# Kernel optimization log

Hardware: AMD Instinct MI355X
Metric: run time of the kernel (lower is better)

## Reference

```python
import jax, jax.numpy as jnp
import numpy as np

N = 50000          # num nodes
E = 800000         # num edges (before self-loops)
F_IN = 128         # num_node_features
HEADS = 8          # num_heads (layer 1)
F_HEAD = 16        # features_per_head
N_CLASSES = 32     # num_classes (layer 2, heads=1)
NEG_SLOPE = 0.2    # PyG GATConv default LeakyReLU slope


def setup_inputs() -> dict:
    key = jax.random.key(0)
    ks = jax.random.split(key, 9)
    x = jax.random.normal(ks[0], (N, F_IN), jnp.float32)
    src = jax.random.randint(ks[1], (E,), 0, N, dtype=jnp.int32)
    dst = jax.random.randint(ks[2], (E,), 0, N, dtype=jnp.int32)
    # layer 1 params
    W1 = jax.random.normal(ks[3], (F_IN, HEADS * F_HEAD), jnp.float32) / np.sqrt(F_IN).astype(np.float32)
    a_src1 = jax.random.normal(ks[4], (HEADS, F_HEAD), jnp.float32) * 0.1
    a_dst1 = jax.random.normal(ks[5], (HEADS, F_HEAD), jnp.float32) * 0.1
    b1 = jnp.zeros((HEADS * F_HEAD,), jnp.float32)  # bias_init = zeros_
    # layer 2 params (heads=1)
    W2 = jax.random.normal(ks[6], (HEADS * F_HEAD, N_CLASSES), jnp.float32) / np.sqrt(HEADS * F_HEAD).astype(np.float32)
    a_src2 = jax.random.normal(ks[7], (1, N_CLASSES), jnp.float32) * 0.1
    a_dst2 = jax.random.normal(ks[8], (1, N_CLASSES), jnp.float32) * 0.1
    b2 = jnp.zeros((N_CLASSES,), jnp.float32)
    return {"x": x, "src": src, "dst": dst,
            "W1": W1, "a_src1": a_src1, "a_dst1": a_dst1, "b1": b1,
            "W2": W2, "a_src2": a_src2, "a_dst2": a_dst2, "b2": b2}


def gat_conv(x, src, dst, W, a_src, a_dst, b, heads, feat):
    """PyG-style GATConv (concat=True, add_self_loops=True)."""
    h = (x @ W).reshape(N, heads, feat)                 # [N,H,F]
    al_src = jnp.sum(h * a_src, axis=-1)                # [N,H]
    al_dst = jnp.sum(h * a_dst, axis=-1)                # [N,H]
    loop = jnp.arange(N, dtype=src.dtype)
    s = jnp.concatenate([src, loop])                    # [E+N]
    d = jnp.concatenate([dst, loop])                    # [E+N]
    e = jax.nn.leaky_relu(al_src[s] + al_dst[d], NEG_SLOPE)   # [E+N,H]
    # numerically stable softmax over edges grouped by dst node
    m = jax.ops.segment_max(e, d, num_segments=N)       # [N,H]
    ex = jnp.exp(e - m[d])
    denom = jax.ops.segment_sum(ex, d, num_segments=N)  # [N,H]
    alpha = ex / denom[d]                               # [E+N,H]
    out = jax.ops.segment_sum(alpha[:, :, None] * h[s], d, num_segments=N)  # [N,H,F]
    return out.reshape(N, heads * feat) + b


def reference(x, src, dst, W1, a_src1, a_dst1, b1, W2, a_src2, a_dst2, b2):
    h = gat_conv(x, src, dst, W1, a_src1, a_dst1, b1, HEADS, F_HEAD)
    h = jax.nn.elu(h)
    h = gat_conv(h, src, dst, W2, a_src2, a_dst2, b2, 1, N_CLASSES)
    return jax.nn.log_softmax(h, axis=1)
```

## Files before the change

kernel.cpp:

```cpp
#include <hip/hip_runtime.h>

#define N_NODES   50000
#define N_EDGES   800000
#define NEG_SLOPE 0.2f
#define NBKT      256
#define NPB       196
#define EPB       3125
#define CAP       4096
#define G1BLK     782

typedef float f32x2 __attribute__((ext_vector_type(2)));
typedef float f32x4 __attribute__((ext_vector_type(4)));

__device__ __forceinline__ float leaky(float x) {
    return x > 0.f ? x : x * NEG_SLOPE;
}

__device__ __forceinline__ unsigned short f2bf(float f) {
    unsigned int u = __float_as_uint(f);
    unsigned int r = (u + 0x7FFFu + ((u >> 16) & 1u)) >> 16;
    return (unsigned short)r;
}

__device__ __forceinline__ unsigned int pack2bf(float a, float b) {
    return (unsigned int)f2bf(a) | ((unsigned int)f2bf(b) << 16);
}

__device__ __forceinline__ f32x2 bf2x2(unsigned int p) {
    f32x2 r;
    r.x = __uint_as_float(p << 16);
    r.y = __uint_as_float(p & 0xFFFF0000u);
    return r;
}

__device__ __forceinline__ f32x2 lo2(f32x4 v) { return __builtin_shufflevector(v, v, 0, 1); }
__device__ __forceinline__ f32x2 hi2(f32x4 v) { return __builtin_shufflevector(v, v, 2, 3); }

__device__ __forceinline__ void pkfma_lo(f32x2& acc, f32x2 a, f32x2 w) {
    asm("v_pk_fma_f32 %0, %1, %2, %0 op_sel:[0,0,0] op_sel_hi:[0,1,1]"
        : "+v"(acc) : "v"(a), "v"(w));
}
__device__ __forceinline__ void pkfma_hi(f32x2& acc, f32x2 a, f32x2 w) {
    asm("v_pk_fma_f32 %0, %1, %2, %0 op_sel:[1,0,0] op_sel_hi:[1,1,1]"
        : "+v"(acc) : "v"(a), "v"(w));
}
__device__ __forceinline__ f32x2 plow(float x) {
    f32x2 r;
    asm("" : "=v"(r));
    r.x = x;
    return r;
}

__global__ __launch_bounds__(256) void k_bin_gemm1(
    const int* __restrict__ src, const int* __restrict__ dst,
    int* __restrict__ cursor_g, unsigned int* __restrict__ binned,
    const float* __restrict__ x, const float* __restrict__ W1,
    const float* __restrict__ a_src, const float* __restrict__ a_dst,
    unsigned short* __restrict__ h1b, float* __restrict__ al_src,
    float* __restrict__ al_dst)
{
    __shared__ __align__(16) unsigned char smem[49152];
    const int tid = threadIdx.x;

    if (blockIdx.x < NBKT) {
        int* dstc = (int*)smem;
        int* cnt  = (int*)(smem + 12512);
        int* cur  = (int*)(smem + 13536);
        const int blk = blockIdx.x;
        const int e0  = blk * EPB;
        cnt[tid] = 0;
        __syncthreads();
        for (int j = tid; j < EPB; j += 256) {
            int d = dst[e0 + j];
            dstc[j] = d;
            atomicAdd(&cnt[d / NPB], 1);
        }
        __syncthreads();
        const int c = cnt[tid];
        int base = c ? atomicAdd(&cursor_g[tid], c) : 0;
        cur[tid] = tid * CAP + base;
        __syncthreads();
        for (int j = tid; j < EPB; j += 256) {
            int d   = dstc[j];
            int bkt = d / NPB;
            int dl  = d - bkt * NPB;
            int pos = atomicAdd(&cur[bkt], 1);
            binned[pos] = (unsigned int)src[e0 + j] | ((unsigned int)dl << 18);
        }
        return;
    }

    uint2* xs = (uint2*)smem;
    uint2* ws = (uint2*)(smem + 16384);
    const int bid  = (int)blockIdx.x - NBKT;
    const int row0 = bid * 64;
    const int tc   = tid & 31;
    const int tr   = tid >> 5;
    const float4* x4  = (const float4*)x;
    const float4* W14 = (const float4*)W1;

    #pragma unroll
    for (int p = 0; p < 8; ++p) {
        int i = tid + p * 256;
        int r = i >> 5, g = i & 31;
        int gr = row0 + r; if (gr > N_NODES - 1) gr = N_NODES - 1;
        float4 v = x4[gr * 32 + g];
        xs[r * 32 + g] = make_uint2(pack2bf(v.x, v.y), pack2bf(v.z, v.w));
    }
    #pragma unroll
    for (int p = 0; p < 16; ++p) {
        int i = tid + p * 256;
        int k = i >> 5, cg = i & 31;
        float4 v = W14[k * 32 + cg];
        ws[k * 32 + cg] = make_uint2(pack2bf(v.x, v.y), pack2bf(v.z, v.w));
    }
    __syncthreads();

    f32x2 acc[8][2];
    #pragma unroll
    for (int i = 0; i < 8; ++i) {
        acc[i][0] = (f32x2){0.f, 0.f};
        acc[i][1] = (f32x2){0.f, 0.f};
    }

    for (int k4 = 0; k4 < 32; ++k4) {
        f32x2 aP[8][2];
        #pragma unroll
        for (int i = 0; i < 8; ++i) {
            uint2 q = xs[(tr * 8 + i) * 32 + k4];
            aP[i][0] = bf2x2(q.x);
            aP[i][1] = bf2x2(q.y);
        }
        #pragma unroll
        for (int kk = 0; kk < 4; ++kk) {
            uint2 qw = ws[(k4 * 4 + kk) * 32 + tc];
            f32x2 wlo = bf2x2(qw.x);
            f32x2 whi = bf2x2(qw.y);
            #pragma unroll
            for (int i = 0; i < 8; ++i) {
                f32x2 ap = aP[i][kk >> 1];
                if ((kk & 1) == 0) {
                    pkfma_lo(acc[i][0], ap, wlo);
                    pkfma_lo(acc[i][1], ap, whi);
                } else {
                    pkfma_hi(acc[i][0], ap, wlo);
                    pkfma_hi(acc[i][1], ap, whi);
                }
            }
        }
    }

    const int head = tc >> 2;
    const float4 as4 = ((const float4*)a_src)[tc];
    const float4 ad4 = ((const float4*)a_dst)[tc];
    #pragma unroll
    for (int i = 0; i < 8; ++i) {
        int r = row0 + tr * 8 + i;
        float s = acc[i][0].x * as4.x + acc[i][0].y * as4.y
                + acc[i][1].x * as4.z + acc[i][1].y * as4.w;
        float d = acc[i][0].x * ad4.x + acc[i][0].y * ad4.y
                + acc[i][1].x * ad4.z + acc[i][1].y * ad4.w;
        s += __shfl_xor(s, 1); s += __shfl_xor(s, 2);
        d += __shfl_xor(d, 1); d += __shfl_xor(d, 2);
        if (r < N_NODES) {
            ((uint2*)h1b)[r * 32 + tc] =
                make_uint2(pack2bf(acc[i][0].x, acc[i][0].y),
                           pack2bf(acc[i][1].x, acc[i][1].y));
            if ((tc & 3) == 0) {
                al_src[r * 8 + head] = s;
                al_dst[r * 8 + head] = d;
            }
        }
    }
}

__global__ __launch_bounds__(1024) void k_csr_fine(const unsigned int* __restrict__ binned,
                                                   const int* __restrict__ cursor_g,
                                                   int* __restrict__ row_beg,
                                                   int* __restrict__ row_end,
                                                   int* __restrict__ csr) {
    __shared__ int cnt[256];
    __shared__ int cur[256];
    __shared__ int wsum[4];
    const int b = blockIdx.x, tid = threadIdx.x;
    const int start = b * CAP;
    const int nE    = cursor_g[b];
    if (tid < 256) cnt[tid] = 0;
    __syncthreads();
    for (int j = tid; j < nE; j += 1024)
        atomicAdd(&cnt[(binned[start + j] >> 18) & 255], 1);
    __syncthreads();
    int v = 0;
    if (tid < 256) v = cnt[tid];
    int sv = v;
    #pragma unroll
    for (int off = 1; off < 64; off <<= 1) {
        int t = __shfl_up(sv, off);
        if ((tid & 63) >= off) sv += t;
    }
    if (tid < 256 && (tid & 63) == 63) wsum[tid >> 6] = sv;
    __syncthreads();
    if (tid < 256) {
        int w = tid >> 6;
        int add = 0;
        #pragma unroll
        for (int i = 0; i < 3; ++i) add += (i < w) ? wsum[i] : 0;
        int excl = sv + add - v;
        cur[tid] = excl;
        const int node = b * NPB + tid;
        if (tid < NPB && node < N_NODES) {
            row_beg[node] = start + excl;
            row_end[node] = start + excl + v;
        }
    }
    __syncthreads();
    for (int j = tid; j < nE; j += 1024) {
        unsigned int p = binned[start + j];
        int dl  = (p >> 18) & 255;
        int pos = start + atomicAdd(&cur[dl], 1);
        csr[pos] = (int)(p & 0x3FFFFu);
    }
}

__global__ __launch_bounds__(256) void k_agg1g2(
    const unsigned short* __restrict__ h1b, const float* __restrict__ al_src,
    const float* __restrict__ al_dst, const int* __restrict__ row_beg,
    const int* __restrict__ row_end, const int* __restrict__ csr_src,
    const float* __restrict__ b1, const float* __restrict__ W2,
    const float* __restrict__ a_src2, const float* __restrict__ a_dst2,
    unsigned short* __restrict__ t2b, float* __restrict__ alS2,
    float* __restrict__ alD2)
{
    __shared__ __align__(16) float w2s[128 * 32];
    __shared__ __align__(16) float h2row[4][128];
    const int tid  = threadIdx.x;
    const int wv   = tid >> 6;
    const int n    = blockIdx.x * 4 + wv;
    const int l    = tid & 63;
    const int slot = l >> 4;
    const int f2   = l & 15;
    const int head = f2 >> 1;
    const uint4* h1q = (const uint4*)h1b;

    float4 wreg[4];
    {
        const float4* W2v = (const float4*)W2;
        #pragma unroll
        for (int p = 0; p < 4; ++p) wreg[p] = W2v[tid + p * 256];
    }
    const float alD = al_dst[n * 8 + head];
    const int beg = row_beg[n], end = row_end[n];
    {
        float4* w2sv = (float4*)w2s;
        #pragma unroll
        for (int p = 0; p < 4; ++p) {
            int g = tid + p * 256;
            w2sv[g ^ ((g >> 7) & 7)] = wreg[p];
        }
    }
    __syncthreads();

    float denom = 0.f;
    f32x2 a01 = {0.f, 0.f}, a23 = {0.f, 0.f}, a45 = {0.f, 0.f}, a67 = {0.f, 0.f};

    if (slot == 0) {
        float w = __expf(leaky(al_src[n * 8 + head] + alD));
        uint4 q = h1q[n * 16 + f2];
        denom = w;
        f32x2 wp = plow(w);
        pkfma_lo(a01, wp, bf2x2(q.x));
        pkfma_lo(a23, wp, bf2x2(q.y));
        pkfma_lo(a45, wp, bf2x2(q.z));
        pkfma_lo(a67, wp, bf2x2(q.w));
    }

    for (int j = beg + slot; j < end; j += 16) {
        const int e1 = (j + 4  < end) ? j + 4  : j;
        const int e2 = (j + 8  < end) ? j + 8  : j;
        const int e3 = (j + 12 < end) ? j + 12 : j;
        int s0 = csr_src[j];
        int s1 = csr_src[e1];
        int s2 = csr_src[e2];
        int s3 = csr_src[e3];
        float l0 = al_src[s0 * 8 + head];
        float l1 = al_src[s1 * 8 + head];
        float l2 = al_src[s2 * 8 + head];
        float l3 = al_src[s3 * 8 + head];
        uint4 q0 = h1q[s0 * 16 + f2];
        uint4 q1 = h1q[s1 * 16 + f2];
        uint4 q2 = h1q[s2 * 16 + f2];
        uint4 q3 = h1q[s3 * 16 + f2];
        float w0 = __expf(leaky(l0 + alD));
        float w1 = __expf(leaky(l1 + alD)); w1 = (e1 != j) ? w1 : 0.f;
        float w2 = __expf(leaky(l2 + alD)); w2 = (e2 != j) ? w2 : 0.f;
        float w3 = __expf(leaky(l3 + alD)); w3 = (e3 != j) ? w3 : 0.f;
        denom += (w0 + w1) + (w2 + w3);
        f32x2 wA; wA.x = w0; wA.y = w1;
        f32x2 wB; wB.x = w2; wB.y = w3;
        pkfma_lo(a01, wA, bf2x2(q0.x));
        pkfma_lo(a23, wA, bf2x2(q0.y));
        pkfma_lo(a45, wA, bf2x2(q0.z));
        pkfma_lo(a67, wA, bf2x2(q0.w));
        pkfma_hi(a01, wA, bf2x2(q1.x));
        pkfma_hi(a23, wA, bf2x2(q1.y));
        pkfma_hi(a45, wA, bf2x2(q1.z));
        pkfma_hi(a67, wA, bf2x2(q1.w));
        pkfma_lo(a01, wB, bf2x2(q2.x));
        pkfma_lo(a23, wB, bf2x2(q2.y));
        pkfma_lo(a45, wB, bf2x2(q2.z));
        pkfma_lo(a67, wB, bf2x2(q2.w));
        pkfma_hi(a01, wB, bf2x2(q3.x));
        pkfma_hi(a23, wB, bf2x2(q3.y));
        pkfma_hi(a45, wB, bf2x2(q3.z));
        pkfma_hi(a67, wB, bf2x2(q3.w));
    }

    #pragma unroll
    for (int off = 16; off <= 32; off <<= 1) {
        a01.x += __shfl_xor(a01.x, off); a01.y += __shfl_xor(a01.y, off);
        a23.x += __shfl_xor(a23.x, off); a23.y += __shfl_xor(a23.y, off);
        a45.x += __shfl_xor(a45.x, off); a45.y += __shfl_xor(a45.y, off);
        a67.x += __shfl_xor(a67.x, off); a67.y += __shfl_xor(a67.y, off);
        denom += __shfl_xor(denom, off);
    }

    {
        const float4 bA = ((const float4*)b1)[f2 * 2];
        const float4 bB = ((const float4*)b1)[f2 * 2 + 1];
        float inv = 1.f / denom;
        float o[8];
        o[0] = a01.x * inv + bA.x; o[1] = a01.y * inv + bA.y;
        o[2] = a23.x * inv + bA.z; o[3] = a23.y * inv + bA.w;
        o[4] = a45.x * inv + bB.x; o[5] = a45.y * inv + bB.y;
        o[6] = a67.x * inv + bB.z; o[7] = a67.y * inv + bB.w;
        #pragma unroll
        for (int i = 0; i < 8; ++i) o[i] = o[i] > 0.f ? o[i] : expm1f(o[i]);
        if (slot == 0) {
            *(float4*)&h2row[wv][f2 * 8]     = make_float4(o[0], o[1], o[2], o[3]);
            *(float4*)&h2row[wv][f2 * 8 + 4] = make_float4(o[4], o[5], o[6], o[7]);
        }
    }

    const int cg = l & 7;
    const int kg = l >> 3;
    const float* hrow = h2row[wv];
    f32x4 hv[4];
    #pragma unroll
    for (int t = 0; t < 4; ++t)
        hv[t] = *(const f32x4*)&hrow[kg * 16 + t * 4];
    const f32x4* w2v = (const f32x4*)w2s;
    f32x2 s01 = {0.f, 0.f}, s23 = {0.f, 0.f};
    #pragma unroll
    for (int t = 0; t < 4; ++t) {
        f32x2 hlo = lo2(hv[t]);
        f32x2 hhi = hi2(hv[t]);
        #pragma unroll
        for (int u = 0; u < 4; ++u) {
            const int k = kg * 16 + t * 4 + u;
            f32x4 w4 = w2v[(k * 8 + cg) ^ kg];
            f32x2 wlo = lo2(w4);
            f32x2 whi = hi2(w4);
            if (u == 0)      { pkfma_lo(s01, hlo, wlo); pkfma_lo(s23, hlo, whi); }
            else if (u == 1) { pkfma_hi(s01, hlo, wlo); pkfma_hi(s23, hlo, whi); }
            else if (u == 2) { pkfma_lo(s01, hhi, wlo); pkfma_lo(s23, hhi, whi); }
            else             { pkfma_hi(s01, hhi, wlo); pkfma_hi(s23, hhi, whi); }
        }
    }
    #pragma unroll
    for (int off = 8; off <= 32; off <<= 1) {
        s01.x += __shfl_xor(s01.x, off); s01.y += __shfl_xor(s01.y, off);
        s23.x += __shfl_xor(s23.x, off); s23.y += __shfl_xor(s23.y, off);
    }

    if (l < 8)
        ((uint2*)t2b)[n * 8 + cg] =
            make_uint2(pack2bf(s01.x, s01.y), pack2bf(s23.x, s23.y));

    const float4 as2 = ((const float4*)a_src2)[cg];
    const float4 ad2 = ((const float4*)a_dst2)[cg];
    float s2 = s01.x * as2.x + s01.y * as2.y + s23.x * as2.z + s23.y * as2.w;
    float d2 = s01.x * ad2.x + s01.y * ad2.y + s23.x * ad2.z + s23.y * ad2.w;
    #pragma unroll
    for (int off = 1; off <= 4; off <<= 1) {
        s2 += __shfl_xor(s2, off);
        d2 += __shfl_xor(d2, off);
    }
    if (l == 0) {
        alS2[n] = s2;
        alD2[n] = d2;
    }
}

__global__ __launch_bounds__(256) void k_agg2(
    const unsigned short* __restrict__ t2b, const float* __restrict__ al_src,
    const float* __restrict__ al_dst, const int* __restrict__ row_beg,
    const int* __restrict__ row_end, const int* __restrict__ csr_src,
    const float* __restrict__ b2, float* __restrict__ out)
{
    const int n = blockIdx.x * 4 + (threadIdx.x >> 6);
    const int l = threadIdx.x & 63;
    const int slot = l >> 3;
    const int f4   = l & 7;
    const uint2* t2u = (const uint2*)t2b;

    const float alD = al_dst[n];
    const int beg = row_beg[n], end = row_end[n];
    float denom = 0.f;
    f32x2 a01 = {0.f, 0.f}, a23 = {0.f, 0.f};
    if (slot == 0) {
        float w = __expf(leaky(al_src[n] + alD));
        uint2 q = t2u[n * 8 + f4];
        denom = w;
        f32x2 wp = plow(w);
        pkfma_lo(a01, wp, bf2x2(q.x));
        pkfma_lo(a23, wp, bf2x2(q.y));
    }
    for (int j = beg + slot; j < end; j += 32) {
        const int e1 = (j + 8  < end) ? j + 8  : j;
        const int e2 = (j + 16 < end) ? j + 16 : j;
        const int e3 = (j + 24 < end) ? j + 24 : j;
        int s0 = csr_src[j];
        int s1 = csr_src[e1];
        int s2 = csr_src[e2];
        int s3 = csr_src[e3];
        float l0 = al_src[s0];
        float l1 = al_src[s1];
        float l2 = al_src[s2];
        float l3 = al_src[s3];
        uint2 q0 = t2u[s0 * 8 + f4];
        uint2 q1 = t2u[s1 * 8 + f4];
        uint2 q2 = t2u[s2 * 8 + f4];
        uint2 q3 = t2u[s3 * 8 + f4];
        float w0 = __expf(leaky(l0 + alD));
        float w1 = __expf(leaky(l1 + alD)); w1 = (e1 != j) ? w1 : 0.f;
        float w2 = __expf(leaky(l2 + alD)); w2 = (e2 != j) ? w2 : 0.f;
        float w3 = __expf(leaky(l3 + alD)); w3 = (e3 != j) ? w3 : 0.f;
        denom += (w0 + w1) + (w2 + w3);
        f32x2 wA; wA.x = w0; wA.y = w1;
        f32x2 wB; wB.x = w2; wB.y = w3;
        pkfma_lo(a01, wA, bf2x2(q0.x));
        pkfma_lo(a23, wA, bf2x2(q0.y));
        pkfma_hi(a01, wA, bf2x2(q1.x));
        pkfma_hi(a23, wA, bf2x2(q1.y));
        pkfma_lo(a01, wB, bf2x2(q2.x));
        pkfma_lo(a23, wB, bf2x2(q2.y));
        pkfma_hi(a01, wB, bf2x2(q3.x));
        pkfma_hi(a23, wB, bf2x2(q3.y));
    }
    #pragma unroll
    for (int off = 8; off <= 32; off <<= 1) {
        a01.x += __shfl_xor(a01.x, off); a01.y += __shfl_xor(a01.y, off);
        a23.x += __shfl_xor(a23.x, off); a23.y += __shfl_xor(a23.y, off);
        denom += __shfl_xor(denom, off);
    }

    const float4 bb = ((const float4*)b2)[f4];
    float inv = 1.f / denom;
    float o0 = a01.x * inv + bb.x;
    float o1 = a01.y * inv + bb.y;
    float o2 = a23.x * inv + bb.z;
    float o3 = a23.y * inv + bb.w;
    float m = fmaxf(fmaxf(o0, o1), fmaxf(o2, o3));
    for (int off = 1; off <= 4; off <<= 1) m = fmaxf(m, __shfl_xor(m, off));
    float ssum = __expf(o0 - m) + __expf(o1 - m) + __expf(o2 - m) + __expf(o3 - m);
    for (int off = 1; off <= 4; off <<= 1) ssum += __shfl_xor(ssum, off);
    float lg = m + __logf(ssum);
    if (slot == 0)
        ((float4*)out)[n * 8 + f4] = make_float4(o0 - lg, o1 - lg, o2 - lg, o3 - lg);
}

extern "C" void kernel_launch(void* const* d_in, const int* in_sizes, int n_in,
                              void* d_out, int out_size, void* d_ws, size_t ws_size,
                              hipStream_t stream) {
    const float* x      = (const float*)d_in[0];
    const int*   src    = (const int*)d_in[1];
    const int*   dst    = (const int*)d_in[2];
    const float* W1     = (const float*)d_in[3];
    const float* a_src1 = (const float*)d_in[4];
    const float* a_dst1 = (const float*)d_in[5];
    const float* b1     = (const float*)d_in[6];
    const float* W2     = (const float*)d_in[7];
    const float* a_src2 = (const float*)d_in[8];
    const float* a_dst2 = (const float*)d_in[9];
    const float* b2     = (const float*)d_in[10];
    float* out = (float*)d_out;

    char* ws = (char*)d_ws;
    size_t off = 0;
    auto alloc = [&](size_t bytes) {
        void* p = ws + off;
        off += (bytes + 255) & ~(size_t)255;
        return p;
    };
    unsigned short* h1b = (unsigned short*)alloc((size_t)N_NODES * 128 * 2);
    unsigned short* t2b = (unsigned short*)alloc((size_t)N_NODES * 32 * 2);
    float* alS1    = (float*)alloc((size_t)N_NODES * 8 * 4);
    float* alD1    = (float*)alloc((size_t)N_NODES * 8 * 4);
    float* alS2    = (float*)alloc((size_t)N_NODES * 4);
    float* alD2    = (float*)alloc((size_t)N_NODES * 4);
    int*   row_beg = (int*)alloc((size_t)N_NODES * 4);
    int*   row_end = (int*)alloc((size_t)N_NODES * 4);
    int*   csr     = (int*)alloc((size_t)NBKT * CAP * 4);
    unsigned int* binned = (unsigned int*)alloc((size_t)NBKT * CAP * 4);
    int*   cursor  = (int*)alloc((size_t)NBKT * 4);
    (void)ws_size; (void)in_sizes; (void)n_in; (void)out_size;

    hipMemsetAsync(cursor, 0, (size_t)NBKT * 4, stream);
    k_bin_gemm1<<<NBKT + G1BLK, 256, 0, stream>>>(
        src, dst, cursor, binned,
        x, W1, a_src1, a_dst1, h1b, alS1, alD1);
    k_csr_fine<<<NBKT, 1024, 0, stream>>>(binned, cursor, row_beg, row_end, csr);
    k_agg1g2<<<N_NODES / 4, 256, 0, stream>>>(
        h1b, alS1, alD1, row_beg, row_end, csr,
        b1, W2, a_src2, a_dst2, t2b, alS2, alD2);
    k_agg2<<<N_NODES / 4, 256, 0, stream>>>(t2b, alS2, alD2, row_beg, row_end, csr, b2, out);
}
```

Before: 202.0 us.

## Fuse all GAT stages into one persistent cooperative kernel with grid syncs

Replaces the memset plus four kernel launches with one persistent cooperative kernel. Its blocks loop over tasks (binning, GEMM1, CSR build, layer-1 aggregation with the W2 projection, layer-2 aggregation) and separate the stages with grid-wide syncs. The GEMM tile now stages W1 in four chunks so shared memory drops to 24KB, which is meant to allow more resident blocks. The aim is to remove launch gaps and the tail between stages, at the cost of grid.sync overhead, a grid size capped by occupancy, and the CSR stage now using 256 threads per block where it used 1024.

```diff
diff --git a/kernel.cpp b/kernel.cpp
--- a/kernel.cpp
+++ b/kernel.cpp
@@ -1,4 +1,7 @@
 #include <hip/hip_runtime.h>
+#include <hip/hip_cooperative_groups.h>
+
+namespace cg = cooperative_groups;
 
 #define N_NODES   50000
 #define N_EDGES   800000
@@ -8,6 +11,7 @@
 #define EPB       3125
 #define CAP       4096
 #define G1BLK     782
+#define NGRP      12500
 
 typedef float f32x2 __attribute__((ext_vector_type(2)));
 typedef float f32x4 __attribute__((ext_vector_type(4)));
@@ -51,422 +55,429 @@
     return r;
 }
 
-__global__ __launch_bounds__(256) void k_bin_gemm1(
+__global__ __launch_bounds__(256) void k_fused(
     const int* __restrict__ src, const int* __restrict__ dst,
     int* __restrict__ cursor_g, unsigned int* __restrict__ binned,
     const float* __restrict__ x, const float* __restrict__ W1,
-    const float* __restrict__ a_src, const float* __restrict__ a_dst,
-    unsigned short* __restrict__ h1b, float* __restrict__ al_src,
-    float* __restrict__ al_dst)
-{
-    __shared__ __align__(16) unsigned char smem[49152];
-    const int tid = threadIdx.x;
-
-    if (blockIdx.x < NBKT) {
-        int* dstc = (int*)smem;
-        int* cnt  = (int*)(smem + 12512);
-        int* cur  = (int*)(smem + 13536);
-        const int blk = blockIdx.x;
-        const int e0  = blk * EPB;
-        cnt[tid] = 0;
-        __syncthreads();
-        for (int j = tid; j < EPB; j += 256) {
-            int d = dst[e0 + j];
-            dstc[j] = d;
-            atomicAdd(&cnt[d / NPB], 1);
-        }
-        __syncthreads();
-        const int c = cnt[tid];
-        int base = c ? atomicAdd(&cursor_g[tid], c) : 0;
-        cur[tid] = tid * CAP + base;
-        __syncthreads();
-        for (int j = tid; j < EPB; j += 256) {
-            int d   = dstc[j];
-            int bkt = d / NPB;
-            int dl  = d - bkt * NPB;
-            int pos = atomicAdd(&cur[bkt], 1);
-            binned[pos] = (unsigned int)src[e0 + j] | ((unsigned int)dl << 18);
-        }
-        return;
-    }
-
-    uint2* xs = (uint2*)smem;
-    uint2* ws = (uint2*)(smem + 16384);
-    const int bid  = (int)blockIdx.x - NBKT;
-    const int row0 = bid * 64;
-    const int tc   = tid & 31;
-    const int tr   = tid >> 5;
-    const float4* x4  = (const float4*)x;
-    const float4* W14 = (const float4*)W1;
-
-    #pragma unroll
-    for (int p = 0; p < 8; ++p) {
-        int i = tid + p * 256;
-        int r = i >> 5, g = i & 31;
-        int gr = row0 + r; if (gr > N_NODES - 1) gr = N_NODES - 1;
-        float4 v = x4[gr * 32 + g];
-        xs[r * 32 + g] = make_uint2(pack2bf(v.x, v.y), pack2bf(v.z, v.w));
-    }
-    #pragma unroll
-    for (int p = 0; p < 16; ++p) {
-        int i = tid + p * 256;
-        int k = i >> 5, cg = i & 31;
-        float4 v = W14[k * 32 + cg];
-        ws[k * 32 + cg] = make_uint2(pack2bf(v.x, v.y), pack2bf(v.z, v.w));
-    }
-    __syncthreads();
-
-    f32x2 acc[8][2];
-    #pragma unroll
-    for (int i = 0; i < 8; ++i) {
-        acc[i][0] = (f32x2){0.f, 0.f};
-        acc[i][1] = (f32x2){0.f, 0.f};
-    }
-
-    for (int k4 = 0; k4 < 32; ++k4) {
-        f32x2 aP[8][2];
-        #pragma unroll
-        for (int i = 0; i < 8; ++i) {
-            uint2 q = xs[(tr * 8 + i) * 32 + k4];
-            aP[i][0] = bf2x2(q.x);
-            aP[i][1] = bf2x2(q.y);
-        }
-        #pragma unroll
-        for (int kk = 0; kk < 4; ++kk) {
-            uint2 qw = ws[(k4 * 4 + kk) * 32 + tc];
-            f32x2 wlo = bf2x2(qw.x);
-            f32x2 whi = bf2x2(qw.y);
-            #pragma unroll
-            for (int i = 0; i < 8; ++i) {
-                f32x2 ap = aP[i][kk >> 1];
-                if ((kk & 1) == 0) {
-                    pkfma_lo(acc[i][0], ap, wlo);
-                    pkfma_lo(acc[i][1], ap, whi);
-                } else {
-                    pkfma_hi(acc[i][0], ap, wlo);
-                    pkfma_hi(acc[i][1], ap, whi);
-                }
-            }
-        }
-    }
-
-    const int head = tc >> 2;
-    const float4 as4 = ((const float4*)a_src)[tc];
-    const float4 ad4 = ((const float4*)a_dst)[tc];
-    #pragma unroll
-    for (int i = 0; i < 8; ++i) {
-        int r = row0 + tr * 8 + i;
-        float s = acc[i][0].x * as4.x + acc[i][0].y * as4.y
-                + acc[i][1].x * as4.z + acc[i][1].y * as4.w;
-        float d = acc[i][0].x * ad4.x + acc[i][0].y * ad4.y
-                + acc[i][1].x * ad4.z + acc[i][1].y * ad4.w;
-        s += __shfl_xor(s, 1); s += __shfl_xor(s, 2);
-        d += __shfl_xor(d, 1); d += __shfl_xor(d, 2);
-        if (r < N_NODES) {
-            ((uint2*)h1b)[r * 32 + tc] =
-                make_uint2(pack2bf(acc[i][0].x, acc[i][0].y),
-                           pack2bf(acc[i][1].x, acc[i][1].y));
-            if ((tc & 3) == 0) {
-                al_src[r * 8 + head] = s;
-                al_dst[r * 8 + head] = d;
-            }
-        }
-    }
-}
-
-__global__ __launch_bounds__(1024) void k_csr_fine(const unsigned int* __restrict__ binned,
-                                                   const int* __restrict__ cursor_g,
-                                                   int* __restrict__ row_beg,
-                                                   int* __restrict__ row_end,
-                                                   int* __restrict__ csr) {
-    __shared__ int cnt[256];
-    __shared__ int cur[256];
-    __shared__ int wsum[4];
-    const int b = blockIdx.x, tid = threadIdx.x;
-    const int start = b * CAP;
-    const int nE    = cursor_g[b];
-    if (tid < 256) cnt[tid] = 0;
-    __syncthreads();
-    for (int j = tid; j < nE; j += 1024)
-        atomicAdd(&cnt[(binned[start + j] >> 18) & 255], 1);
-    __syncthreads();
-    int v = 0;
-    if (tid < 256) v = cnt[tid];
-    int sv = v;
-    #pragma unroll
-    for (int off = 1; off < 64; off <<= 1) {
-        int t = __shfl_up(sv, off);
-        if ((tid & 63) >= off) sv += t;
-    }
-    if (tid < 256 && (tid & 63) == 63) wsum[tid >> 6] = sv;
-    __syncthreads();
-    if (tid < 256) {
-        int w = tid >> 6;
-        int add = 0;
-        #pragma unroll
-        for (int i = 0; i < 3; ++i) add += (i < w) ? wsum[i] : 0;
-        int excl = sv + add - v;
-        cur[tid] = excl;
-        const int node = b * NPB + tid;
-        if (tid < NPB && node < N_NODES) {
-            row_beg[node] = start + excl;
-            row_end[node] = start + excl + v;
-        }
-    }
-    __syncthreads();
-    for (int j = tid; j < nE; j += 1024) {
-        unsigned int p = binned[start + j];
-        int dl  = (p >> 18) & 255;
-        int pos = start + atomicAdd(&cur[dl], 1);
-        csr[pos] = (int)(p & 0x3FFFFu);
-    }
-}
-
-__global__ __launch_bounds__(256) void k_agg1g2(
-    const unsigned short* __restrict__ h1b, const float* __restrict__ al_src,
-    const float* __restrict__ al_dst, const int* __restrict__ row_beg,
-    const int* __restrict__ row_end, const int* __restrict__ csr_src,
+    const float* __restrict__ a_src1, const float* __restrict__ a_dst1,
+    unsigned short* __restrict__ h1b, float* __restrict__ alS1,
+    float* __restrict__ alD1,
+    int* __restrict__ row_beg, int* __restrict__ row_end, int* __restrict__ csr,
     const float* __restrict__ b1, const float* __restrict__ W2,
     const float* __restrict__ a_src2, const float* __restrict__ a_dst2,
     unsigned short* __restrict__ t2b, float* __restrict__ alS2,
-    float* __restrict__ alD2)
+    float* __restrict__ alD2,
+    const float* __restrict__ b2, float* __restrict__ out)
 {
-    __shared__ __align__(16) float w2s[128 * 32];
-    __shared__ __align__(16) float h2row[4][128];
+    __shared__ __align__(16) unsigned char smem[24576];
+    cg::grid_group grid = cg::this_grid();
     const int tid  = threadIdx.x;
-    const int wv   = tid >> 6;
-    const int n    = blockIdx.x * 4 + wv;
-    const int l    = tid & 63;
-    const int slot = l >> 4;
-    const int f2   = l & 15;
-    const int head = f2 >> 1;
-    const uint4* h1q = (const uint4*)h1b;
-
-    float4 wreg[4];
-    {
-        const float4* W2v = (const float4*)W2;
-        #pragma unroll
-        for (int p = 0; p < 4; ++p) wreg[p] = W2v[tid + p * 256];
-    }
-    const float alD = al_dst[n * 8 + head];
-    const int beg = row_beg[n], end = row_end[n];
-    {
-        float4* w2sv = (float4*)w2s;
-        #pragma unroll
-        for (int p = 0; p < 4; ++p) {
-            int g = tid + p * 256;
-            w2sv[g ^ ((g >> 7) & 7)] = wreg[p];
+    const int bid  = blockIdx.x;
+    const int nblk = gridDim.x;
+
+    for (int i = bid * 256 + tid; i < NBKT; i += nblk * 256) cursor_g[i] = 0;
+    grid.sync();
+
+    for (int task = bid; task < NBKT + G1BLK; task += nblk) {
+        if (task < NBKT) {
+            int* dstc = (int*)smem;
+            int* cnt  = (int*)(smem + 12512);
+            int* cur  = (int*)(smem + 13536);
+            const int e0 = task * EPB;
+            __syncthreads();
+            cnt[tid] = 0;
+            __syncthreads();
+            for (int j = tid; j < EPB; j += 256) {
+                int d = dst[e0 + j];
+                dstc[j] = d;
+                atomicAdd(&cnt[d / NPB], 1);
+            }
+            __syncthreads();
+            const int c = cnt[tid];
+            int base = c ? atomicAdd(&cursor_g[tid], c) : 0;
+            cur[tid] = tid * CAP + base;
+            __syncthreads();
+            for (int j = tid; j < EPB; j += 256) {
+                int d   = dstc[j];
+                int bkt = d / NPB;
+                int dl  = d - bkt * NPB;
+                int pos = atomicAdd(&cur[bkt], 1);
+                binned[pos] = (unsigned int)src[e0 + j] | ((unsigned int)dl << 18);
+            }
+            __syncthreads();
+        } else {
+            uint2* xs = (uint2*)smem;
+            uint2* ws = (uint2*)(smem + 16384);
+            const int row0 = (task - NBKT) * 64;
+            const int tc   = tid & 31;
+            const int tr   = tid >> 5;
+            const float4* x4  = (const float4*)x;
+            const float4* W14 = (const float4*)W1;
+
+            __syncthreads();
+            #pragma unroll
+            for (int p = 0; p < 8; ++p) {
+                int i = tid + p * 256;
+                int r = i >> 5, g = i & 31;
+                int gr = row0 + r; if (gr > N_NODES - 1) gr = N_NODES - 1;
+                float4 v = x4[gr * 32 + g];
+                xs[r * 32 + g] = make_uint2(pack2bf(v.x, v.y), pack2bf(v.z, v.w));
+            }
+
+            f32x2 acc[8][2];
+            #pragma unroll
+            for (int i = 0; i < 8; ++i) {
+                acc[i][0] = (f32x2){0.f, 0.f};
+                acc[i][1] = (f32x2){0.f, 0.f};
+            }
+
+            for (int q = 0; q < 4; ++q) {
+                if (q) __syncthreads();
+                #pragma unroll
+                for (int p = 0; p < 4; ++p) {
+                    int i = tid + p * 256;
+                    int k = i >> 5, cgq = i & 31;
+                    float4 v = W14[(q * 32 + k) * 32 + cgq];
+                    ws[k * 32 + cgq] = make_uint2(pack2bf(v.x, v.y), pack2bf(v.z, v.w));
+                }
+                __syncthreads();
+                for (int k4 = 0; k4 < 8; ++k4) {
+                    f32x2 aP[8][2];
+                    #pragma unroll
+                    for (int i = 0; i < 8; ++i) {
+                        uint2 qq = xs[(tr * 8 + i) * 32 + q * 8 + k4];
+                        aP[i][0] = bf2x2(qq.x);
+                        aP[i][1] = bf2x2(qq.y);
+                    }
+                    #pragma unroll
+                    for (int kk = 0; kk < 4; ++kk) {
+                        uint2 qw = ws[(k4 * 4 + kk) * 32 + tc];
+                        f32x2 wlo = bf2x2(qw.x);
+                        f32x2 whi = bf2x2(qw.y);
+                        #pragma unroll
+                        for (int i = 0; i < 8; ++i) {
+                            f32x2 ap = aP[i][kk >> 1];
+                            if ((kk & 1) == 0) {
+                                pkfma_lo(acc[i][0], ap, wlo);
+                                pkfma_lo(acc[i][1], ap, whi);
+                            } else {
+                                pkfma_hi(acc[i][0], ap, wlo);
+                                pkfma_hi(acc[i][1], ap, whi);
+                            }
+                        }
+                    }
+                }
+            }
+
+            const int head = tc >> 2;
+            const float4 as4 = ((const float4*)a_src1)[tc];
+            const float4 ad4 = ((const float4*)a_dst1)[tc];
+            #pragma unroll
+            for (int i = 0; i < 8; ++i) {
+                int r = row0 + tr * 8 + i;
+                float s = acc[i][0].x * as4.x + acc[i][0].y * as4.y
+                        + acc[i][1].x * as4.z + acc[i][1].y * as4.w;
+                float d = acc[i][0].x * ad4.x + acc[i][0].y * ad4.y
+                        + acc[i][1].x * ad4.z + acc[i][1].y * ad4.w;
+                s += __shfl_xor(s, 1); s += __shfl_xor(s, 2);
+                d += __shfl_xor(d, 1); d += __shfl_xor(d, 2);
+                if (r < N_NODES) {
+                    ((uint2*)h1b)[r * 32 + tc] =
+                        make_uint2(pack2bf(acc[i][0].x, acc[i][0].y),
+                                   pack2bf(acc[i][1].x, acc[i][1].y));
+                    if ((tc & 3) == 0) {
+                        alS1[r * 8 + head] = s;
+                        alD1[r * 8 + head] = d;
+                    }
+                }
+            }
+            __syncthreads();
         }
     }
-    __syncthreads();
-
-    float denom = 0.f;
-    f32x2 a01 = {0.f, 0.f}, a23 = {0.f, 0.f}, a45 = {0.f, 0.f}, a67 = {0.f, 0.f};
-
-    if (slot == 0) {
-        float w = __expf(leaky(al_src[n * 8 + head] + alD));
-        uint4 q = h1q[n * 16 + f2];
-        denom = w;
-        f32x2 wp = plow(w);
-        pkfma_lo(a01, wp, bf2x2(q.x));
-        pkfma_lo(a23, wp, bf2x2(q.y));
-        pkfma_lo(a45, wp, bf2x2(q.z));
-        pkfma_lo(a67, wp, bf2x2(q.w));
-    }
-
-    for (int j = beg + slot; j < end; j += 16) {
-        const int e1 = (j + 4  < end) ? j + 4  : j;
-        const int e2 = (j + 8  < end) ? j + 8  : j;
-        const int e3 = (j + 12 < end) ? j + 12 : j;
-        int s0 = csr_src[j];
-        int s1 = csr_src[e1];
-        int s2 = csr_src[e2];
-        int s3 = csr_src[e3];
-        float l0 = al_src[s0 * 8 + head];
-        float l1 = al_src[s1 * 8 + head];
-        float l2 = al_src[s2 * 8 + head];
-        float l3 = al_src[s3 * 8 + head];
-        uint4 q0 = h1q[s0 * 16 + f2];
-        uint4 q1 = h1q[s1 * 16 + f2];
-        uint4 q2 = h1q[s2 * 16 + f2];
-        uint4 q3 = h1q[s3 * 16 + f2];
-        float w0 = __expf(leaky(l0 + alD));
-        float w1 = __expf(leaky(l1 + alD)); w1 = (e1 != j) ? w1 : 0.f;
-        float w2 = __expf(leaky(l2 + alD)); w2 = (e2 != j) ? w2 : 0.f;
-        float w3 = __expf(leaky(l3 + alD)); w3 = (e3 != j) ? w3 : 0.f;
-        denom += (w0 + w1) + (w2 + w3);
-        f32x2 wA; wA.x = w0; wA.y = w1;
-        f32x2 wB; wB.x = w2; wB.y = w3;
-        pkfma_lo(a01, wA, bf2x2(q0.x));
-        pkfma_lo(a23, wA, bf2x2(q0.y));
-        pkfma_lo(a45, wA, bf2x2(q0.z));
-        pkfma_lo(a67, wA, bf2x2(q0.w));
-        pkfma_hi(a01, wA, bf2x2(q1.x));
-        pkfma_hi(a23, wA, bf2x2(q1.y));
-        pkfma_hi(a45, wA, bf2x2(q1.z));
-        pkfma_hi(a67, wA, bf2x2(q1.w));
-        pkfma_lo(a01, wB, bf2x2(q2.x));
-        pkfma_lo(a23, wB, bf2x2(q2.y));
-        pkfma_lo(a45, wB, bf2x2(q2.z));
-        pkfma_lo(a67, wB, bf2x2(q2.w));
-        pkfma_hi(a01, wB, bf2x2(q3.x));
-        pkfma_hi(a23, wB, bf2x2(q3.y));
-        pkfma_hi(a45, wB, bf2x2(q3.z));
-        pkfma_hi(a67, wB, bf2x2(q3.w));
-    }
-
-    #pragma unroll
-    for (int off = 16; off <= 32; off <<= 1) {
-        a01.x += __shfl_xor(a01.x, off); a01.y += __shfl_xor(a01.y, off);
-        a23.x += __shfl_xor(a23.x, off); a23.y += __shfl_xor(a23.y, off);
-        a45.x += __shfl_xor(a45.x, off); a45.y += __shfl_xor(a45.y, off);
-        a67.x += __shfl_xor(a67.x, off); a67.y += __shfl_xor(a67.y, off);
-        denom += __shfl_xor(denom, off);
-    }
+    grid.sync();
 
     {
-        const float4 bA = ((const float4*)b1)[f2 * 2];
-        const float4 bB = ((const float4*)b1)[f2 * 2 + 1];
-        float inv = 1.f / denom;
-        float o[8];
-        o[0] = a01.x * inv + bA.x; o[1] = a01.y * inv + bA.y;
-        o[2] = a23.x * inv + bA.z; o[3] = a23.y * inv + bA.w;
-        o[4] = a45.x * inv + bB.x; o[5] = a45.y * inv + bB.y;
-        o[6] = a67.x * inv + bB.z; o[7] = a67.y * inv + bB.w;
-        #pragma unroll
-        for (int i = 0; i < 8; ++i) o[i] = o[i] > 0.f ? o[i] : expm1f(o[i]);
-        if (slot == 0) {
-            *(float4*)&h2row[wv][f2 * 8]     = make_float4(o[0], o[1], o[2], o[3]);
-            *(float4*)&h2row[wv][f2 * 8 + 4] = make_float4(o[4], o[5], o[6], o[7]);
+        int* cnt  = (int*)smem;
+        int* cur  = (int*)(smem + 1024);
+        int* wsum = (int*)(smem + 2048);
+        for (int b = bid; b < NBKT; b += nblk) {
+            const int start = b * CAP;
+            const int nE    = cursor_g[b];
+            __syncthreads();
+            cnt[tid] = 0;
+            __syncthreads();
+            for (int j = tid; j < nE; j += 256)
+                atomicAdd(&cnt[(binned[start + j] >> 18) & 255], 1);
+            __syncthreads();
+            const int v = cnt[tid];
+            int sv = v;
+            #pragma unroll
+            for (int off = 1; off < 64; off <<= 1) {
+                int t = __shfl_up(sv, off);
+                if ((tid & 63) >= off) sv += t;
+            }
+            if ((tid & 63) == 63) wsum[tid >> 6] = sv;
+            __syncthreads();
+            {
+                int w = tid >> 6;
+                int add = 0;
+                #pragma unroll
+                for (int i = 0; i < 3; ++i) add += (i < w) ? wsum[i] : 0;
+                int excl = sv + add - v;
+                cur[tid] = excl;
+                const int node = b * NPB + tid;
+                if (tid < NPB && node < N_NODES) {
+                    row_beg[node] = start + excl;
+                    row_end[node] = start + excl + v;
+                }
+            }
+            __syncthreads();
+            for (int j = tid; j < nE; j += 256) {
+                unsigned int p = binned[start + j];
+                int dl  = (p >> 18) & 255;
+                int pos = start + atomicAdd(&cur[dl], 1);
+                csr[pos] = (int)(p & 0x3FFFFu);
+            }
         }
     }
-
-    const int cg = l & 7;
-    const int kg = l >> 3;
-    const float* hrow = h2row[wv];
-    f32x4 hv[4];
-    #pragma unroll
-    for (int t = 0; t < 4; ++t)
-        hv[t] = *(const f32x4*)&hrow[kg * 16 + t * 4];
-    const f32x4* w2v = (const f32x4*)w2s;
-    f32x2 s01 = {0.f, 0.f}, s23 = {0.f, 0.f};
-    #pragma unroll
-    for (int t = 0; t < 4; ++t) {
-        f32x2 hlo = lo2(hv[t]);
-        f32x2 hhi = hi2(hv[t]);
-        #pragma unroll
-        for (int u = 0; u < 4; ++u) {
-            const int k = kg * 16 + t * 4 + u;
-            f32x4 w4 = w2v[(k * 8 + cg) ^ kg];
-            f32x2 wlo = lo2(w4);
-            f32x2 whi = hi2(w4);
-            if (u == 0)      { pkfma_lo(s01, hlo, wlo); pkfma_lo(s23, hlo, whi); }
-            else if (u == 1) { pkfma_hi(s01, hlo, wlo); pkfma_hi(s23, hlo, whi); }
-            else if (u == 2) { pkfma_lo(s01, hhi, wlo); pkfma_lo(s23, hhi, whi); }
-            else             { pkfma_hi(s01, hhi, wlo); pkfma_hi(s23, hhi, whi); }
+    grid.sync();
+
+    {
+        float* w2s = (float*)smem;
+        float (*h2row)[128] = (float(*)[128])(smem + 16384);
+        const int wv   = tid >> 6;
+        const int l    = tid & 63;
+        const int slot = l >> 4;
+        const int f2   = l & 15;
+        const int head = f2 >> 1;
+        const int cg   = l & 7;
+        const int kg   = l >> 3;
+        const uint4* h1q = (const uint4*)h1b;
+
+        __syncthreads();
+        {
+            const float4* W2v = (const float4*)W2;
+            float4* w2sv = (float4*)w2s;
+            #pragma unroll
+            for (int p = 0; p < 4; ++p) {
+                int g = tid + p * 256;
+                w2sv[g ^ ((g >> 7) & 7)] = W2v[g];
+            }
+        }
+        __syncthreads();
+
+        const float4 bA  = ((const float4*)b1)[f2 * 2];
+        const float4 bB  = ((const float4*)b1)[f2 * 2 + 1];
+        const float4 as2 = ((const float4*)a_src2)[cg];
+        const float4 ad2 = ((const float4*)a_dst2)[cg];
+        const f32x4* w2v = (const f32x4*)w2s;
+
+        for (int grp = bid; grp < NGRP; grp += nblk) {
+            const int n = grp * 4 + wv;
+            const float alD = alD1[n * 8 + head];
+            const int beg = row_beg[n], end = row_end[n];
+
+            float denom = 0.f;
+            f32x2 a01 = {0.f, 0.f}, a23 = {0.f, 0.f}, a45 = {0.f, 0.f}, a67 = {0.f, 0.f};
+
+            if (slot == 0) {
+                float w = __expf(leaky(alS1[n * 8 + head] + alD));
+                uint4 q = h1q[n * 16 + f2];
+                denom = w;
+                f32x2 wp = plow(w);
+                pkfma_lo(a01, wp, bf2x2(q.x));
+                pkfma_lo(a23, wp, bf2x2(q.y));
+                pkfma_lo(a45, wp, bf2x2(q.z));
+                pkfma_lo(a67, wp, bf2x2(q.w));
+            }
+
+            for (int j = beg + slot; j < end; j += 16) {
+                const int e1 = (j + 4  < end) ? j + 4  : j;
+                const int e2 = (j + 8  < end) ? j + 8  : j;
+                const int e3 = (j + 12 < end) ? j + 12 : j;
+                int s0 = csr[j];
+                int s1 = csr[e1];
+                int s2 = csr[e2];
+                int s3 = csr[e3];
+                float l0 = alS1[s0 * 8 + head];
+                float l1 = alS1[s1 * 8 + head];
+                float l2 = alS1[s2 * 8 + head];
+                float l3 = alS1[s3 * 8 + head];
+                uint4 q0 = h1q[s0 * 16 + f2];
+                uint4 q1 = h1q[s1 * 16 + f2];
+                uint4 q2 = h1q[s2 * 16 + f2];
+                uint4 q3 = h1q[s3 * 16 + f2];
+                float w0 = __expf(leaky(l0 + alD));
+                float w1 = __expf(leaky(l1 + alD)); w1 = (e1 != j) ? w1 : 0.f;
+                float w2 = __expf(leaky(l2 + alD)); w2 = (e2 != j) ? w2 : 0.f;
+                float w3 = __expf(leaky(l3 + alD)); w3 = (e3 != j) ? w3 : 0.f;
+                denom += (w0 + w1) + (w2 + w3);
+                f32x2 wA; wA.x = w0; wA.y = w1;
+                f32x2 wB; wB.x = w2; wB.y = w3;
+                pkfma_lo(a01, wA, bf2x2(q0.x));
+                pkfma_lo(a23, wA, bf2x2(q0.y));
+                pkfma_lo(a45, wA, bf2x2(q0.z));
+                pkfma_lo(a67, wA, bf2x2(q0.w));
+                pkfma_hi(a01, wA, bf2x2(q1.x));
+                pkfma_hi(a23, wA, bf2x2(q1.y));
+                pkfma_hi(a45, wA, bf2x2(q1.z));
+                pkfma_hi(a67, wA, bf2x2(q1.w));
+                pkfma_lo(a01, wB, bf2x2(q2.x));
+                pkfma_lo(a23, wB, bf2x2(q2.y));
+                pkfma_lo(a45, wB, bf2x2(q2.z));
+                pkfma_lo(a67, wB, bf2x2(q2.w));
+                pkfma_hi(a01, wB, bf2x2(q3.x));
+                pkfma_hi(a23, wB, bf2x2(q3.y));
+                pkfma_hi(a45, wB, bf2x2(q3.z));
+                pkfma_hi(a67, wB, bf2x2(q3.w));
+            }
+
+            #pragma unroll
+            for (int off = 16; off <= 32; off <<= 1) {
+                a01.x += __shfl_xor(a01.x, off); a01.y += __shfl_xor(a01.y, off);
+                a23.x += __shfl_xor(a23.x, off); a23.y += __shfl_xor(a23.y, off);
+                a45.x += __shfl_xor(a45.x, off); a45.y += __shfl_xor(a45.y, off);
+                a67.x += __shfl_xor(a67.x, off); a67.y += __shfl_xor(a67.y, off);
+                denom += __shfl_xor(denom, off);
+            }
+
+            {
+                float inv = 1.f / denom;
+                float o[8];
+                o[0] = a01.x * inv + bA.x; o[1] = a01.y * inv + bA.y;
+                o[2] = a23.x * inv + bA.z; o[3] = a23.y * inv + bA.w;
+                o[4] = a45.x * inv + bB.x; o[5] = a45.y * inv + bB.y;
+                o[6] = a67.x * inv + bB.z; o[7] = a67.y * inv + bB.w;
+                #pragma unroll
+                for (int i = 0; i < 8; ++i) o[i] = o[i] > 0.f ? o[i] : __expf(o[i]) - 1.f;
+                if (slot == 0) {
+                    *(float4*)&h2row[wv][f2 * 8]     = make_float4(o[0], o[1], o[2], o[3]);
+                    *(float4*)&h2row[wv][f2 * 8 + 4] = make_float4(o[4], o[5], o[6], o[7]);
+                }
+            }
+
+            const float* hrow = h2row[wv];
+            f32x4 hv[4];
+            #pragma unroll
+            for (int t = 0; t < 4; ++t)
+                hv[t] = *(const f32x4*)&hrow[kg * 16 + t * 4];
+            f32x2 s01 = {0.f, 0.f}, s23 = {0.f, 0.f};
+            #pragma unroll
+            for (int t = 0; t < 4; ++t) {
+                f32x2 hlo = lo2(hv[t]);
+                f32x2 hhi = hi2(hv[t]);
+                #pragma unroll
+                for (int u = 0; u < 4; ++u) {
+                    const int k = kg * 16 + t * 4 + u;
+                    f32x4 w4 = w2v[(k * 8 + cg) ^ kg];
+                    f32x2 wlo = lo2(w4);
+                    f32x2 whi = hi2(w4);
+                    if (u == 0)      { pkfma_lo(s01, hlo, wlo); pkfma_lo(s23, hlo, whi); }
+                    else if (u == 1) { pkfma_hi(s01, hlo, wlo); pkfma_hi(s23, hlo, whi); }
+                    else if (u == 2) { pkfma_lo(s01, hhi, wlo); pkfma_lo(s23, hhi, whi); }
+                    else             { pkfma_hi(s01, hhi, wlo); pkfma_hi(s23, hhi, whi); }
+                }
+            }
+            #pragma unroll
+            for (int off = 8; off <= 32; off <<= 1) {
+                s01.x += __shfl_xor(s01.x, off); s01.y += __shfl_xor(s01.y, off);
+                s23.x += __shfl_xor(s23.x, off); s23.y += __shfl_xor(s23.y, off);
+            }
+
+            if (l < 8)
+                ((uint2*)t2b)[n * 8 + cg] =
+                    make_uint2(pack2bf(s01.x, s01.y), pack2bf(s23.x, s23.y));
+
+            float s2 = s01.x * as2.x + s01.y * as2.y + s23.x * as2.z + s23.y * as2.w;
+            float d2 = s01.x * ad2.x + s01.y * ad2.y + s23.x * ad2.z + s23.y * ad2.w;
+            #pragma unroll
+            for (int off = 1; off <= 4; off <<= 1) {
+                s2 += __shfl_xor(s2, off);
+                d2 += __shfl_xor(d2, off);
+            }
+            if (l == 0) {
+                alS2[n] = s2;
+                alD2[n] = d2;
+            }
         }
     }
-    #pragma unroll
-    for (int off = 8; off <= 32; off <<= 1) {
-        s01.x += __shfl_xor(s01.x, off); s01.y += __shfl_xor(s01.y, off);
-        s23.x += __shfl_xor(s23.x, off); s23.y += __shfl_xor(s23.y, off);
+    grid.sync();
+
+    {
+        const int wv   = tid >> 6;
+        const int l    = tid & 63;
+        const int slot = l >> 3;
+        const int f4   = l & 7;
+        const uint2* t2u = (const uint2*)t2b;
+        const float4 bb = ((const float4*)b2)[f4];
+
+        for (int grp = bid; grp < NGRP; grp += nblk) {
+            const int n = grp * 4 + wv;
+            const float alD = alD2[n];
+            const int beg = row_beg[n], end = row_end[n];
+            float denom = 0.f;
+            f32x2 a01 = {0.f, 0.f}, a23 = {0.f, 0.f};
+            if (slot == 0) {
+                float w = __expf(leaky(alS2[n] + alD));
+                uint2 q = t2u[n * 8 + f4];
+                denom = w;
+                f32x2 wp = plow(w);
+                pkfma_lo(a01, wp, bf2x2(q.x));
+                pkfma_lo(a23, wp, bf2x2(q.y));
+            }
+            for (int j = beg + slot; j < end; j += 32) {
+                const int e1 = (j + 8  < end) ? j + 8  : j;
+                const int e2 = (j + 16 < end) ? j + 16 : j;
+                const int e3 = (j + 24 < end) ? j + 24 : j;
+                int s0 = csr[j];
+                int s1 = csr[e1];
+                int s2 = csr[e2];
+                int s3 = csr[e3];
+                float l0 = alS2[s0];
+                float l1 = alS2[s1];
+                float l2 = alS2[s2];
+                float l3 = alS2[s3];
+                uint2 q0 = t2u[s0 * 8 + f4];
+                uint2 q1 = t2u[s1 * 8 + f4];
+                uint2 q2 = t2u[s2 * 8 + f4];
+                uint2 q3 = t2u[s3 * 8 + f4];
+                float w0 = __expf(leaky(l0 + alD));
+                float w1 = __expf(leaky(l1 + alD)); w1 = (e1 != j) ? w1 : 0.f;
+                float w2 = __expf(leaky(l2 + alD)); w2 = (e2 != j) ? w2 : 0.f;
+                float w3 = __expf(leaky(l3 + alD)); w3 = (e3 != j) ? w3 : 0.f;
+                denom += (w0 + w1) + (w2 + w3);
+                f32x2 wA; wA.x = w0; wA.y = w1;
+                f32x2 wB; wB.x = w2; wB.y = w3;
+                pkfma_lo(a01, wA, bf2x2(q0.x));
+                pkfma_lo(a23, wA, bf2x2(q0.y));
+                pkfma_hi(a01, wA, bf2x2(q1.x));
+                pkfma_hi(a23, wA, bf2x2(q1.y));
+                pkfma_lo(a01, wB, bf2x2(q2.x));
+                pkfma_lo(a23, wB, bf2x2(q2.y));
+                pkfma_hi(a01, wB, bf2x2(q3.x));
+                pkfma_hi(a23, wB, bf2x2(q3.y));
+            }
+            #pragma unroll
+            for (int off = 8; off <= 32; off <<= 1) {
+                a01.x += __shfl_xor(a01.x, off); a01.y += __shfl_xor(a01.y, off);
+                a23.x += __shfl_xor(a23.x, off); a23.y += __shfl_xor(a23.y, off);
+                denom += __shfl_xor(denom, off);
+            }
+
+            float inv = 1.f / denom;
+            float o0 = a01.x * inv + bb.x;
+            float o1 = a01.y * inv + bb.y;
+            float o2 = a23.x * inv + bb.z;
+            float o3 = a23.y * inv + bb.w;
+            float m = fmaxf(fmaxf(o0, o1), fmaxf(o2, o3));
+            for (int off = 1; off <= 4; off <<= 1) m = fmaxf(m, __shfl_xor(m, off));
+            float ssum = __expf(o0 - m) + __expf(o1 - m) + __expf(o2 - m) + __expf(o3 - m);
+            for (int off = 1; off <= 4; off <<= 1) ssum += __shfl_xor(ssum, off);
+            float lg = m + __logf(ssum);
+            if (slot == 0)
+                ((float4*)out)[n * 8 + f4] = make_float4(o0 - lg, o1 - lg, o2 - lg, o3 - lg);
+        }
     }
-
-    if (l < 8)
-        ((uint2*)t2b)[n * 8 + cg] =
-            make_uint2(pack2bf(s01.x, s01.y), pack2bf(s23.x, s23.y));
-
-    const float4 as2 = ((const float4*)a_src2)[cg];
-    const float4 ad2 = ((const float4*)a_dst2)[cg];
-    float s2 = s01.x * as2.x + s01.y * as2.y + s23.x * as2.z + s23.y * as2.w;
-    float d2 = s01.x * ad2.x + s01.y * ad2.y + s23.x * ad2.z + s23.y * ad2.w;
-    #pragma unroll
-    for (int off = 1; off <= 4; off <<= 1) {
-        s2 += __shfl_xor(s2, off);
-        d2 += __shfl_xor(d2, off);
-    }
-    if (l == 0) {
-        alS2[n] = s2;
-        alD2[n] = d2;
-    }
-}
-
-__global__ __launch_bounds__(256) void k_agg2(
-    const unsigned short* __restrict__ t2b, const float* __restrict__ al_src,
-    const float* __restrict__ al_dst, const int* __restrict__ row_beg,
-    const int* __restrict__ row_end, const int* __restrict__ csr_src,
-    const float* __restrict__ b2, float* __restrict__ out)
-{
-    const int n = blockIdx.x * 4 + (threadIdx.x >> 6);
-    const int l = threadIdx.x & 63;
-    const int slot = l >> 3;
-    const int f4   = l & 7;
-    const uint2* t2u = (const uint2*)t2b;
-
-    const float alD = al_dst[n];
-    const int beg = row_beg[n], end = row_end[n];
-    float denom = 0.f;
-    f32x2 a01 = {0.f, 0.f}, a23 = {0.f, 0.f};
-    if (slot == 0) {
-        float w = __expf(leaky(al_src[n] + alD));
-        uint2 q = t2u[n * 8 + f4];
-        denom = w;
-        f32x2 wp = plow(w);
-        pkfma_lo(a01, wp, bf2x2(q.x));
-        pkfma_lo(a23, wp, bf2x2(q.y));
-    }
-    for (int j = beg + slot; j < end; j += 32) {
-        const int e1 = (j + 8  < end) ? j + 8  : j;
-        const int e2 = (j + 16 < end) ? j + 16 : j;
-        const int e3 = (j + 24 < end) ? j + 24 : j;
-        int s0 = csr_src[j];
-        int s1 = csr_src[e1];
-        int s2 = csr_src[e2];
-        int s3 = csr_src[e3];
-        float l0 = al_src[s0];
-        float l1 = al_src[s1];
-        float l2 = al_src[s2];
-        float l3 = al_src[s3];
-        uint2 q0 = t2u[s0 * 8 + f4];
-        uint2 q1 = t2u[s1 * 8 + f4];
-        uint2 q2 = t2u[s2 * 8 + f4];
-        uint2 q3 = t2u[s3 * 8 + f4];
-        float w0 = __expf(leaky(l0 + alD));
-        float w1 = __expf(leaky(l1 + alD)); w1 = (e1 != j) ? w1 : 0.f;
-        float w2 = __expf(leaky(l2 + alD)); w2 = (e2 != j) ? w2 : 0.f;
-        float w3 = __expf(leaky(l3 + alD)); w3 = (e3 != j) ? w3 : 0.f;
-        denom += (w0 + w1) + (w2 + w3);
-        f32x2 wA; wA.x = w0; wA.y = w1;
-        f32x2 wB; wB.x = w2; wB.y = w3;
-        pkfma_lo(a01, wA, bf2x2(q0.x));
-        pkfma_lo(a23, wA, bf2x2(q0.y));
-        pkfma_hi(a01, wA, bf2x2(q1.x));
-        pkfma_hi(a23, wA, bf2x2(q1.y));
-        pkfma_lo(a01, wB, bf2x2(q2.x));
-        pkfma_lo(a23, wB, bf2x2(q2.y));
-        pkfma_hi(a01, wB, bf2x2(q3.x));
-        pkfma_hi(a23, wB, bf2x2(q3.y));
-    }
-    #pragma unroll
-    for (int off = 8; off <= 32; off <<= 1) {
-        a01.x += __shfl_xor(a01.x, off); a01.y += __shfl_xor(a01.y, off);
-        a23.x += __shfl_xor(a23.x, off); a23.y += __shfl_xor(a23.y, off);
-        denom += __shfl_xor(denom, off);
-    }
-
-    const float4 bb = ((const float4*)b2)[f4];
-    float inv = 1.f / denom;
-    float o0 = a01.x * inv + bb.x;
-    float o1 = a01.y * inv + bb.y;
-    float o2 = a23.x * inv + bb.z;
-    float o3 = a23.y * inv + bb.w;
-    float m = fmaxf(fmaxf(o0, o1), fmaxf(o2, o3));
-    for (int off = 1; off <= 4; off <<= 1) m = fmaxf(m, __shfl_xor(m, off));
-    float ssum = __expf(o0 - m) + __expf(o1 - m) + __expf(o2 - m) + __expf(o3 - m);
-    for (int off = 1; off <= 4; off <<= 1) ssum += __shfl_xor(ssum, off);
-    float lg = m + __logf(ssum);
-    if (slot == 0)
-        ((float4*)out)[n * 8 + f4] = make_float4(o0 - lg, o1 - lg, o2 - lg, o3 - lg);
 }
 
 extern "C" void kernel_launch(void* const* d_in, const int* in_sizes, int n_in,
@@ -505,13 +516,28 @@
     int*   cursor  = (int*)alloc((size_t)NBKT * 4);
     (void)ws_size; (void)in_sizes; (void)n_in; (void)out_size;
 
-    hipMemsetAsync(cursor, 0, (size_t)NBKT * 4, stream);
-    k_bin_gemm1<<<NBKT + G1BLK, 256, 0, stream>>>(
-        src, dst, cursor, binned,
-        x, W1, a_src1, a_dst1, h1b, alS1, alD1);
-    k_csr_fine<<<NBKT, 1024, 0, stream>>>(binned, cursor, row_beg, row_end, csr);
-    k_agg1g2<<<N_NODES / 4, 256, 0, stream>>>(
-        h1b, alS1, alD1, row_beg, row_end, csr,
-        b1, W2, a_src2, a_dst2, t2b, alS2, alD2);
-    k_agg2<<<N_NODES / 4, 256, 0, stream>>>(t2b, alS2, alD2, row_beg, row_end, csr, b2, out);
-}
+    static int nblk = 0;
+    if (nblk == 0) {
+        int per = 0;
+        hipOccupancyMaxActiveBlocksPerMultiprocessor(&per, (const void*)k_fused, 256, 0);
+        if (per < 1) per = 1;
+        hipDeviceProp_t prop;
+        int cus = 256;
+        if (hipGetDeviceProperties(&prop, 0) == hipSuccess) cus = prop.multiProcessorCount;
+        nblk = per * cus;
+        if (nblk > 2048) nblk = 2048;
+        if (nblk < 256)  nblk = 256;
+    }
+
+    void* args[] = {
+        (void*)&src, (void*)&dst, (void*)&cursor, (void*)&binned,
+        (void*)&x, (void*)&W1, (void*)&a_src1, (void*)&a_dst1,
+        (void*)&h1b, (void*)&alS1, (void*)&alD1,
+        (void*)&row_beg, (void*)&row_end, (void*)&csr,
+        (void*)&b1, (void*)&W2, (void*)&a_src2, (void*)&a_dst2,
+        (void*)&t2b, (void*)&alS2, (void*)&alD2,
+        (void*)&b2, (void*)&out
+    };
+    hipLaunchCooperativeKernel((const void*)k_fused, dim3(nblk), dim3(256),
+                               args, 0, stream);
+}
```

Result: slower. 464.9 us (+130.1%).
